# Kernel tuning notes

Hardware: AMD Instinct MI355X
Metric: run time of the kernel (lower is better)

## Reference

```python
import jax, jax.numpy as jnp
import numpy as np

K = 3        # kernel_size
STRIDE = 1
DIL = 1

N, C_X, H, W = 16, 512, 64, 64
C_W = 64  # weight channels; groups = C_X // C_W = 8 (share_planes)


def setup_inputs() -> dict:
    key = jax.random.key(0)
    k1, k2 = jax.random.split(key)
    inp = jax.random.normal(k1, (N, C_X, H, W), dtype=jnp.float32)
    # weight: [n, c_w, k^2, out_h*out_w]
    weight = jax.random.normal(k2, (N, C_W, K * K, H * W), dtype=jnp.float32)
    return {"input": inp, "weight": weight}


def reference(input, weight):
    n, c_x, in_h, in_w = input.shape
    c_w = weight.shape[1]
    groups = c_x // c_w
    pad = (DIL * (K - 1) + 1) // 2
    out_h = (in_h + 2 * pad - (DIL * (K - 1) + 1)) // STRIDE + 1
    out_w = (in_w + 2 * pad - (DIL * (K - 1) + 1)) // STRIDE + 1

    # zero-pad spatial dims (aggregation_zeropad semantics)
    xp = jnp.pad(input, ((0, 0), (0, 0), (pad, pad), (pad, pad)))
    # weight -> [n, 1, c_w, k^2, out_h, out_w] for broadcast over group axis
    wr = weight.reshape(n, 1, c_w, K * K, out_h, out_w)

    # Fused per-kernel-offset gather-multiply-accumulate: avoids materializing
    # the full [n, c_x, k^2, L] im2col tensor the TF code builds.
    acc = jnp.zeros((n, groups, c_w, out_h, out_w), dtype=input.dtype)
    for i in range(K):
        for j in range(K):
            patch = xp[:, :,
                       i * DIL:i * DIL + STRIDE * out_h:STRIDE,
                       j * DIL:j * DIL + STRIDE * out_w:STRIDE]
            acc = acc + patch.reshape(n, groups, c_w, out_h, out_w) * wr[:, :, :, i * K + j]
    return acc.reshape(n, c_x, out_h, out_w)
```

## Files before the change

### kernel.cpp

```cpp
#include <hip/hip_runtime.h>


#define HW 4096
#define CX 512
#define CW 64
#define NGRP 8

__global__ __launch_bounds__(256) void agg_kernel(const float* __restrict__ in,
                                                  const float* __restrict__ wgt,
                                                  float* __restrict__ out)
{
    const int bid = blockIdx.x;
    const int yt  = bid & 3;
    const int nc  = bid >> 2;
    const int c   = nc & 63;
    const int n   = nc >> 6;

    const int tid = threadIdx.x;
    const int qx  = tid & 15;
    const int yl  = tid >> 4;
    const int y   = yt * 16 + yl;
    const int x0  = qx * 4;

    const float* wbase = wgt + ((size_t)(n * CW + c) * 9) * HW + y * 64 + x0;
    float4 w[9];
#pragma unroll
    for (int t = 0; t < 9; ++t)
        w[t] = *reinterpret_cast<const float4*>(wbase + (size_t)t * HW);

    const size_t nc_off = (size_t)n * CX * HW + (size_t)c * HW;
    const float* inb  = in  + nc_off;
    float*       outb = out + nc_off + (size_t)y * 64 + x0;

#pragma unroll
    for (int g = 0; g < NGRP; ++g) {
        const float* plane = inb + (size_t)g * CW * HW;
        float4 acc = make_float4(0.f, 0.f, 0.f, 0.f);
#pragma unroll
        for (int i = 0; i < 3; ++i) {
            const int ry = y + i - 1;
            float4 v;
            float lft, rgt;
            if (ry >= 0 && ry < 64) {
                const float* row = plane + ry * 64;
                v   = *reinterpret_cast<const float4*>(row + x0);
                lft = (x0 > 0)      ? row[x0 - 1] : 0.f;
                rgt = (x0 + 4 < 64) ? row[x0 + 4] : 0.f;
            } else {
                v = make_float4(0.f, 0.f, 0.f, 0.f);
                lft = 0.f; rgt = 0.f;
            }
            const float4 lv = make_float4(lft, v.x, v.y, v.z);
            const float4 rv = make_float4(v.y, v.z, v.w, rgt);
            const float4 w0 = w[i * 3 + 0];
            const float4 w1 = w[i * 3 + 1];
            const float4 w2 = w[i * 3 + 2];
            acc.x += lv.x * w0.x + v.x * w1.x + rv.x * w2.x;
            acc.y += lv.y * w0.y + v.y * w1.y + rv.y * w2.y;
            acc.z += lv.z * w0.z + v.z * w1.z + rv.z * w2.z;
            acc.w += lv.w * w0.w + v.w * w1.w + rv.w * w2.w;
        }
        *reinterpret_cast<float4*>(outb + (size_t)g * CW * HW) = acc;
    }
}

extern "C" void kernel_launch(void* const* d_in, const int* in_sizes, int n_in,
                              void* d_out, int out_size, void* d_ws, size_t ws_size,
                              hipStream_t stream) {
    const float* in  = (const float*)d_in[0];
    const float* wg  = (const float*)d_in[1];
    float*       out = (float*)d_out;
    agg_kernel<<<4096, 256, 0, stream>>>(in, wg, out);
}
```

Before: 349.4 us.

## Replace halo scalar loads with wave shuffles and double-buffer group row loads

Each thread now gets its left and right halo values from neighbouring lanes with width-16 shuffles instead of two extra scalar global loads per row. The three row float4 loads for the next group are issued before the current group is computed, using a two-slot register buffer. FMA chains are written out explicitly. This cuts the number of load instructions and overlaps memory latency with compute, at the cost of more registers and changed summation order.

```diff
diff --git a/kernel.cpp b/kernel.cpp
--- a/kernel.cpp
+++ b/kernel.cpp
@@ -29,37 +29,71 @@
         w[t] = *reinterpret_cast<const float4*>(wbase + (size_t)t * HW);
 
     const size_t nc_off = (size_t)n * CX * HW + (size_t)c * HW;
-    const float* inb  = in  + nc_off;
+    const float* inb  = in  + nc_off + (size_t)y * 64 + x0;
     float*       outb = out + nc_off + (size_t)y * 64 + x0;
+
+    const bool has_top = (y > 0);
+    const bool has_bot = (y < 63);
+    const float4 zero = make_float4(0.f, 0.f, 0.f, 0.f);
+
+    float4 r0[2], r1[2], r2[2];
+
+    {
+        const float* p = inb;
+        r1[0] = *reinterpret_cast<const float4*>(p);
+        r0[0] = has_top ? *reinterpret_cast<const float4*>(p - 64) : zero;
+        r2[0] = has_bot ? *reinterpret_cast<const float4*>(p + 64) : zero;
+    }
 
 #pragma unroll
     for (int g = 0; g < NGRP; ++g) {
-        const float* plane = inb + (size_t)g * CW * HW;
-        float4 acc = make_float4(0.f, 0.f, 0.f, 0.f);
-#pragma unroll
-        for (int i = 0; i < 3; ++i) {
-            const int ry = y + i - 1;
-            float4 v;
-            float lft, rgt;
-            if (ry >= 0 && ry < 64) {
-                const float* row = plane + ry * 64;
-                v   = *reinterpret_cast<const float4*>(row + x0);
-                lft = (x0 > 0)      ? row[x0 - 1] : 0.f;
-                rgt = (x0 + 4 < 64) ? row[x0 + 4] : 0.f;
-            } else {
-                v = make_float4(0.f, 0.f, 0.f, 0.f);
-                lft = 0.f; rgt = 0.f;
-            }
-            const float4 lv = make_float4(lft, v.x, v.y, v.z);
-            const float4 rv = make_float4(v.y, v.z, v.w, rgt);
-            const float4 w0 = w[i * 3 + 0];
-            const float4 w1 = w[i * 3 + 1];
-            const float4 w2 = w[i * 3 + 2];
-            acc.x += lv.x * w0.x + v.x * w1.x + rv.x * w2.x;
-            acc.y += lv.y * w0.y + v.y * w1.y + rv.y * w2.y;
-            acc.z += lv.z * w0.z + v.z * w1.z + rv.z * w2.z;
-            acc.w += lv.w * w0.w + v.w * w1.w + rv.w * w2.w;
+        const int cur = g & 1;
+        const int nxt = cur ^ 1;
+        if (g < NGRP - 1) {
+            const float* p = inb + (size_t)(g + 1) * CW * HW;
+            r1[nxt] = *reinterpret_cast<const float4*>(p);
+            r0[nxt] = has_top ? *reinterpret_cast<const float4*>(p - 64) : zero;
+            r2[nxt] = has_bot ? *reinterpret_cast<const float4*>(p + 64) : zero;
         }
+
+        float4 a0, a1, a2;
+        {
+            const float4 v = r0[cur];
+            float lft = __shfl_up(v.w, 1, 16);   lft = (qx > 0)  ? lft : 0.f;
+            float rgt = __shfl_down(v.x, 1, 16); rgt = (qx < 15) ? rgt : 0.f;
+            const float4 w0 = w[0], w1 = w[1], w2 = w[2];
+            a0.x = fmaf(lft, w0.x, fmaf(v.x, w1.x, v.y * w2.x));
+            a0.y = fmaf(v.x, w0.y, fmaf(v.y, w1.y, v.z * w2.y));
+            a0.z = fmaf(v.y, w0.z, fmaf(v.z, w1.z, v.w * w2.z));
+            a0.w = fmaf(v.z, w0.w, fmaf(v.w, w1.w, rgt * w2.w));
+        }
+        {
+            const float4 v = r1[cur];
+            float lft = __shfl_up(v.w, 1, 16);   lft = (qx > 0)  ? lft : 0.f;
+            float rgt = __shfl_down(v.x, 1, 16); rgt = (qx < 15) ? rgt : 0.f;
+            const float4 w0 = w[3], w1 = w[4], w2 = w[5];
+            a1.x = fmaf(lft, w0.x, fmaf(v.x, w1.x, v.y * w2.x));
+            a1.y = fmaf(v.x, w0.y, fmaf(v.y, w1.y, v.z * w2.y));
+            a1.z = fmaf(v.y, w0.z, fmaf(v.z, w1.z, v.w * w2.z));
+            a1.w = fmaf(v.z, w0.w, fmaf(v.w, w1.w, rgt * w2.w));
+        }
+        {
+            const float4 v = r2[cur];
+            float lft = __shfl_up(v.w, 1, 16);   lft = (qx > 0)  ? lft : 0.f;
+            float rgt = __shfl_down(v.x, 1, 16); rgt = (qx < 15) ? rgt : 0.f;
+            const float4 w0 = w[6], w1 = w[7], w2 = w[8];
+            a2.x = fmaf(lft, w0.x, fmaf(v.x, w1.x, v.y * w2.x));
+            a2.y = fmaf(v.x, w0.y, fmaf(v.y, w1.y, v.z * w2.y));
+            a2.z = fmaf(v.y, w0.z, fmaf(v.z, w1.z, v.w * w2.z));
+            a2.w = fmaf(v.z, w0.w, fmaf(v.w, w1.w, rgt * w2.w));
+        }
+
+        float4 acc;
+        acc.x = a0.x + a1.x + a2.x;
+        acc.y = a0.y + a1.y + a2.y;
+        acc.z = a0.z + a1.z + a2.z;
+        acc.w = a0.w + a1.w + a2.w;
+
         *reinterpret_cast<float4*>(outb + (size_t)g * CW * HW) = acc;
     }
 }
```

After: 334.7 us. 4.2% less time.
